# Performance work log

Hardware: AMD Instinct MI355X
Metric: run time of the kernel (lower is better)

## Reference

```python
import jax, jax.numpy as jnp
import numpy as np

N = 200000   # nodes
E = 600000   # edges (E*C = 76.8M floats gathered per layer -> memory bound)
C = 128      # channels
L = 2        # GNN layers
OUT = 1      # head out_channels
SEEDS = 1024


def setup_inputs() -> dict:
    key = jax.random.key(0)
    ks = jax.random.split(key, 8)
    s = 1.0 / np.sqrt(C)
    return {
        "x": jax.random.normal(ks[0], (N, C), jnp.float32),
        "node_time": jax.random.randint(ks[1], (N,), 0, 4),          # times in [0,4)
        "edge_index": jax.random.randint(ks[2], (2, E), 0, N),
        "w_root": jax.random.normal(ks[3], (L, C, C), jnp.float32) * s,
        "w_nbr": jax.random.normal(ks[4], (L, C, C), jnp.float32) * s,
        "bias": jnp.zeros((L, C), jnp.float32),
        "ln_g": jnp.ones((L, C), jnp.float32),
        "ln_b": jnp.zeros((L, C), jnp.float32),
        "head_w": jax.random.normal(ks[5], (C, OUT), jnp.float32) * s,
        "head_b": jnp.zeros((OUT,), jnp.float32),
        "min_timestamp": 0,
        "max_timestamp": 3,
        "update_period": 1,
        "num_seeds": SEEDS,
    }


def _layer_norm(h, g, b):
    mu = h.mean(-1, keepdims=True)
    var = h.var(-1, keepdims=True)
    return (h - mu) * jax.lax.rsqrt(var + 1e-5) * g + b


def reference(x, node_time, edge_index, w_root, w_nbr, bias, ln_g, ln_b,
              head_w, head_b, min_timestamp, max_timestamp, update_period, num_seeds):
    src, dst = edge_index[0], edge_index[1]
    n = x.shape[0]
    n_layers = w_root.shape[0]
    # edge introduction time = max of endpoint times (partition_edges_by_time_dict)
    intro = jnp.maximum(node_time[src], node_time[dst])
    periods = (intro - min_timestamp) // update_period
    P = (max_timestamp - min_timestamp + update_period) // update_period  # static int

    for p in range(P):
        emask = periods == p                     # [E] edges of this time period
        ef = emask.astype(x.dtype)
        ei = emask.astype(jnp.int32)
        # nodes involved in this period's subgraph (appear as src or dst of a period edge)
        cnt = jnp.zeros((n,), jnp.int32).at[src].add(ei).at[dst].add(ei)
        involved = cnt > 0                       # [N]
        # in-degree within the period subgraph (for mean aggregation)
        deg = jax.ops.segment_sum(ef, dst, num_segments=n)
        inv_deg = (1.0 / jnp.maximum(deg, 1.0))[:, None]
        # GraphSAGE on the period subgraph: masked edges == subgraph edges, and the
        # per-node (root/LayerNorm/ReLU) transforms agree with the extracted subgraph.
        h = x
        for l in range(n_layers):
            msg = h[src] * ef[:, None]                               # gather + mask
            agg = jax.ops.segment_sum(msg, dst, num_segments=n) * inv_deg
            h = h @ w_root[l] + agg @ w_nbr[l] + bias[l]
            h = _layer_norm(h, ln_g[l], ln_b[l])
            if l < n_layers - 1:
                h = jax.nn.relu(h)
        # x_dict[node_ids] += out_feats  (scatter-add restricted to involved nodes)
        x = x + jnp.where(involved[:, None], h, jnp.zeros((), x.dtype))

    # head: MLP(channels -> out_channels, num_layers=1) on the seed rows
    return x[:num_seeds] @ head_w + head_b
```

## Files before the change

kernel.cpp:

```cpp
#include <hip/hip_runtime.h>


#define CD 128

typedef __attribute__((ext_vector_type(8))) short s16x8;
typedef __attribute__((ext_vector_type(4))) float f32x4;

static __device__ __forceinline__ unsigned short f2bf(float f) {
  unsigned u = __float_as_uint(f);
  u += 0x7FFF + ((u >> 16) & 1);
  return (unsigned short)(u >> 16);
}
static __device__ __forceinline__ float bf2f(unsigned us) {
  return __uint_as_float(us << 16);
}

__global__ __launch_bounds__(256) void histk(const int* __restrict__ ntime,
    const int* __restrict__ eidx, int* __restrict__ deg_pd,
    unsigned char* __restrict__ inv,
    const int* __restrict__ minp, const int* __restrict__ up, int N, int E) {
  int e = blockIdx.x * 256 + threadIdx.x;
  if (e >= E) return;
  int s = eidx[e], d = eidx[E + e];
  int ts = ntime[s], td = ntime[d];
  int m = ts > td ? ts : td;
  int p = (m - minp[0]) / up[0];
  atomicAdd(&deg_pd[p * N + d], 1);
  inv[(size_t)p * N + s] = 1;
  inv[(size_t)p * N + d] = 1;
}

__global__ __launch_bounds__(256) void compcnt(const unsigned char* __restrict__ inv,
    int* __restrict__ bcnt, int NB2, int N) {
  int i = blockIdx.x * 256 + threadIdx.x;
  int bits = 0;
  if (i < N)
    bits = (int)inv[i] | ((int)inv[N + i] << 1)
         | ((int)inv[2 * (size_t)N + i] << 2) | ((int)inv[3 * (size_t)N + i] << 3);
  int wv = threadIdx.x >> 6;
  int lane = threadIdx.x & 63;
  __shared__ int wcnt[4][4];
#pragma unroll
  for (int p = 0; p < 4; ++p) {
    unsigned long long m = __ballot((bits >> p) & 1);
    if (lane == 0) wcnt[p][wv] = __popcll(m);
  }
  __syncthreads();
  if (threadIdx.x < 4) {
    int p = threadIdx.x;
    bcnt[p * NB2 + blockIdx.x] = wcnt[p][0] + wcnt[p][1] + wcnt[p][2] + wcnt[p][3];
  }
}

__global__ __launch_bounds__(256) void compscat(const unsigned char* __restrict__ inv,
    const int* __restrict__ bcnt, const int* __restrict__ bexc,
    int* __restrict__ nlist, int* __restrict__ cidx, int* __restrict__ ncnt,
    int NB2, int N) {
  int i = blockIdx.x * 256 + threadIdx.x;
  int bits = 0;
  if (i < N)
    bits = (int)inv[i] | ((int)inv[N + i] << 1)
         | ((int)inv[2 * (size_t)N + i] << 2) | ((int)inv[3 * (size_t)N + i] << 3);
  if (blockIdx.x == 0 && threadIdx.x < 4) {
    int p = threadIdx.x;
    ncnt[p] = bexc[p * NB2 + NB2 - 1] + bcnt[p * NB2 + NB2 - 1] - bexc[p * NB2];
  }
  int wv = threadIdx.x >> 6;
  int lane = threadIdx.x & 63;
  unsigned long long lanes_below = (lane == 0) ? 0ull : ((~0ull) >> (64 - lane));
  __shared__ int wcnt[4][4];
  unsigned long long mm[4];
#pragma unroll
  for (int p = 0; p < 4; ++p) {
    mm[p] = __ballot((bits >> p) & 1);
    if (lane == 0) wcnt[p][wv] = __popcll(mm[p]);
  }
  __syncthreads();
#pragma unroll
  for (int p = 0; p < 4; ++p) {
    if (!((bits >> p) & 1)) continue;
    int wpre = (wv > 0 ? wcnt[p][0] : 0) + (wv > 1 ? wcnt[p][1] : 0)
             + (wv > 2 ? wcnt[p][2] : 0);
    int base = bexc[p * NB2 + blockIdx.x] - bexc[p * NB2];
    int pos = base + wpre + __popcll(mm[p] & lanes_below);
    nlist[p * N + pos] = i;
    cidx[p * N + i] = pos;
  }
}

__global__ __launch_bounds__(256) void scan1(const int* __restrict__ in,
    int* __restrict__ out, int* __restrict__ bsums, int M) {
  __shared__ int lds[256];
  int tid = threadIdx.x;
  int base = blockIdx.x * 1024 + tid * 4;
  int v0 = base + 0 < M ? in[base + 0] : 0;
  int v1 = base + 1 < M ? in[base + 1] : 0;
  int v2 = base + 2 < M ? in[base + 2] : 0;
  int v3 = base + 3 < M ? in[base + 3] : 0;
  int s = v0 + v1 + v2 + v3;
  lds[tid] = s;
  __syncthreads();
  for (int off = 1; off < 256; off <<= 1) {
    int t = tid >= off ? lds[tid - off] : 0;
    __syncthreads();
    lds[tid] += t;
    __syncthreads();
  }
  int run = lds[tid] - s;
  if (base + 0 < M) out[base + 0] = run; run += v0;
  if (base + 1 < M) out[base + 1] = run; run += v1;
  if (base + 2 < M) out[base + 2] = run; run += v2;
  if (base + 3 < M) out[base + 3] = run;
  if (tid == 255) bsums[blockIdx.x] = lds[255];
}

__global__ __launch_bounds__(256) void scan2(int* __restrict__ b, int M) {
  __shared__ int lds[256];
  int tid = threadIdx.x;
  int base = tid * 4;
  int v0 = base + 0 < M ? b[base + 0] : 0;
  int v1 = base + 1 < M ? b[base + 1] : 0;
  int v2 = base + 2 < M ? b[base + 2] : 0;
  int v3 = base + 3 < M ? b[base + 3] : 0;
  int s = v0 + v1 + v2 + v3;
  lds[tid] = s;
  __syncthreads();
  for (int off = 1; off < 256; off <<= 1) {
    int t = tid >= off ? lds[tid - off] : 0;
    __syncthreads();
    lds[tid] += t;
    __syncthreads();
  }
  int run = lds[tid] - s;
  if (base + 0 < M) b[base + 0] = run; run += v0;
  if (base + 1 < M) b[base + 1] = run; run += v1;
  if (base + 2 < M) b[base + 2] = run; run += v2;
  if (base + 3 < M) b[base + 3] = run;
}

__global__ __launch_bounds__(256) void scan3(int* __restrict__ out,
    const int* __restrict__ bsums, int M) {
  int add = bsums[blockIdx.x];
  int idx = blockIdx.x * 1024 + threadIdx.x;
#pragma unroll
  for (int k = 0; k < 4; ++k) {
    int i = idx + k * 256;
    if (i < M) out[i] += add;
  }
}

__global__ __launch_bounds__(256) void fillk(const int* __restrict__ ntime,
    const int* __restrict__ eidx, int* __restrict__ row_ptr, int* __restrict__ col,
    const int* __restrict__ minp, const int* __restrict__ up, int N, int E) {
  int e = blockIdx.x * 256 + threadIdx.x;
  if (e >= E) return;
  int s = eidx[e], d = eidx[E + e];
  int ts = ntime[s], td = ntime[d];
  int m = ts > td ? ts : td;
  int p = (m - minp[0]) / up[0];
  int pos = atomicAdd(&row_ptr[p * N + d], 1);
  col[pos] = s;
}

__global__ __launch_bounds__(256) void wprep(const float* __restrict__ wroot,
    const float* __restrict__ wnbr, unsigned short* __restrict__ wt, int total) {
  int t = blockIdx.x * 256 + threadIdx.x;
  if (t >= total) return;
  int l = t >> 12;
  int rem = t & 4095;
  int q = rem >> 7;
  int n = rem & 127;
  const float* src = (q < 16) ? (wroot + l * CD * CD) : (wnbr + l * CD * CD);
  int qh = q & 15;
  unsigned short o[8];
#pragma unroll
  for (int j = 0; j < 8; ++j) {
    int kp = qh * 8 + j;
    int kt = (kp & 7) * 16 + (kp >> 3);
    o[j] = f2bf(src[kt * CD + n]);
  }
  uint4 pk;
  pk.x = (unsigned)o[0] | ((unsigned)o[1] << 16);
  pk.y = (unsigned)o[2] | ((unsigned)o[3] << 16);
  pk.z = (unsigned)o[4] | ((unsigned)o[5] << 16);
  pk.w = (unsigned)o[6] | ((unsigned)o[7] << 16);
  *(uint4*)(wt + (size_t)l * 32768 + ((size_t)q * CD + n) * 8) = pk;
}

__global__ __launch_bounds__(256) void xprep(const float* __restrict__ x,
    unsigned short* __restrict__ xb, float* __restrict__ x32, int nseed, int total) {
  int t = blockIdx.x * 256 + threadIdx.x;
  if (t >= total) return;
  int row = t >> 4, j = t & 15;
  const float* xp = x + (size_t)row * CD + j;
  bool seed = row < nseed;
  float* x3 = x32 + (size_t)row * CD + j;
  unsigned short o[8];
#pragma unroll
  for (int tt = 0; tt < 8; ++tt) {
    float v = xp[tt * 16];
    o[tt] = f2bf(v);
    if (seed) x3[tt * 16] = v;
  }
  uint4 pk;
  pk.x = (unsigned)o[0] | ((unsigned)o[1] << 16);
  pk.y = (unsigned)o[2] | ((unsigned)o[3] << 16);
  pk.z = (unsigned)o[4] | ((unsigned)o[5] << 16);
  pk.w = (unsigned)o[6] | ((unsigned)o[7] << 16);
  *(uint4*)(xb + (size_t)row * CD + j * 8) = pk;
}

__global__ __launch_bounds__(256) void aggk(const unsigned short* __restrict__ hbf,
    unsigned short* __restrict__ aggbf, const int* __restrict__ row_ptr,
    const int* __restrict__ deg_pd, const int* __restrict__ col,
    const int* __restrict__ nlp, const int* __restrict__ pcnt,
    const int* __restrict__ cmap, int p, int N) {
  int cnt = pcnt[0];
  int gi = blockIdx.x * 16 + (threadIdx.x >> 4);
  if (gi >= cnt) return;
  int d = nlp[gi];
  int lane = threadIdx.x & 15;
  int key = p * N + d;
  int dg = deg_pd[key];
  uint4 outv = make_uint4(0u, 0u, 0u, 0u);
  if (dg > 0) {
    int start = row_ptr[key] - dg;
    float a[8];
#pragma unroll
    for (int i = 0; i < 8; ++i) a[i] = 0.f;
    for (int j = 0; j < dg; ++j) {
      int s = col[start + j];
      int r = cmap ? cmap[s] : s;
      uint4 rv = *(const uint4*)(hbf + (size_t)r * CD + lane * 8);
      a[0] += bf2f(rv.x & 0xffffu); a[1] += bf2f(rv.x >> 16);
      a[2] += bf2f(rv.y & 0xffffu); a[3] += bf2f(rv.y >> 16);
      a[4] += bf2f(rv.z & 0xffffu); a[5] += bf2f(rv.z >> 16);
      a[6] += bf2f(rv.w & 0xffffu); a[7] += bf2f(rv.w >> 16);
    }
    float sc = 1.0f / (float)dg;
    outv.x = (unsigned)f2bf(a[0] * sc) | ((unsigned)f2bf(a[1] * sc) << 16);
    outv.y = (unsigned)f2bf(a[2] * sc) | ((unsigned)f2bf(a[3] * sc) << 16);
    outv.z = (unsigned)f2bf(a[4] * sc) | ((unsigned)f2bf(a[5] * sc) << 16);
    outv.w = (unsigned)f2bf(a[6] * sc) | ((unsigned)f2bf(a[7] * sc) << 16);
  }
  *(uint4*)(aggbf + (size_t)gi * CD + lane * 8) = outv;
}

__global__ __launch_bounds__(256, 2) void gemm_mfma(
    const unsigned short* __restrict__ A1, const unsigned short* __restrict__ A2,
    const unsigned short* __restrict__ wt,
    const float* __restrict__ bias, const float* __restrict__ lng,
    const float* __restrict__ lnb,
    unsigned short* __restrict__ hout,
    float* __restrict__ x32, unsigned short* __restrict__ xbf,
    const int* __restrict__ nlp, const int* __restrict__ pcnt,
    int mode, int nseed) {
  int cnt = pcnt[0];
  int rbase = blockIdx.x * 128;
  if (rbase >= cnt) return;

  __shared__ unsigned short Blds[32768];
  {
    const uint4* src = (const uint4*)wt;
    uint4* dst = (uint4*)Blds;
#pragma unroll
    for (int i = 0; i < 16; ++i) dst[threadIdx.x + i * 256] = src[threadIdx.x + i * 256];
  }
  __syncthreads();

  int tid = threadIdx.x;
  int w = tid >> 6;
  int lane = tid & 63;
  int l15 = lane & 15;
  int quad = lane >> 4;

  const unsigned short* base1[2];
  const unsigned short* base2[2];
#pragma unroll
  for (int rt = 0; rt < 2; ++rt) {
    int ii = rbase + w * 32 + rt * 16 + l15;
    ii = ii < cnt ? ii : cnt - 1;
    int arow = (mode == 0) ? nlp[ii] : ii;
    base1[rt] = A1 + (size_t)arow * CD;
    base2[rt] = A2 + (size_t)ii * CD;
  }

  s16x8 af[4][2][2];
#pragma unroll
  for (int kc = 0; kc < 4; ++kc) {
    int koff = (kc & 1) * 64;
#pragma unroll
    for (int ks = 0; ks < 2; ++ks) {
      int kb = (ks * 4 + quad) * 8;
#pragma unroll
      for (int rt = 0; rt < 2; ++rt)
        af[kc][ks][rt] = *(const s16x8*)((kc < 2 ? base1[rt] : base2[rt]) + koff + kb);
    }
  }

  f32x4 acc[2][8];
#pragma unroll
  for (int rt = 0; rt < 2; ++rt)
#pragma unroll
    for (int ct = 0; ct < 8; ++ct) acc[rt][ct] = (f32x4)(0.f);

#pragma unroll
  for (int kc = 0; kc < 4; ++kc) {
#pragma unroll
    for (int ks = 0; ks < 2; ++ks) {
      int q = kc * 8 + ks * 4 + quad;
      s16x8 bfr[8];
#pragma unroll
      for (int ct = 0; ct < 8; ++ct)
        bfr[ct] = *(const s16x8*)&Blds[((size_t)q * CD + l15) * 8 + (size_t)ct * 128];
#pragma unroll
      for (int rt = 0; rt < 2; ++rt)
#pragma unroll
        for (int ct = 0; ct < 8; ++ct)
          acc[rt][ct] = __builtin_amdgcn_mfma_f32_16x16x32_bf16(
              af[kc][ks][rt], bfr[ct], acc[rt][ct], 0, 0, 0);
    }
  }

  float bb[8], gg[8], eb[8];
#pragma unroll
  for (int ct = 0; ct < 8; ++ct) {
    int c = ct * 16 + l15;
    bb[ct] = bias[c]; gg[ct] = lng[c]; eb[ct] = lnb[c];
  }
#pragma unroll
  for (int rt = 0; rt < 2; ++rt) {
#pragma unroll
    for (int reg = 0; reg < 4; ++reg) {
      int ridx = rbase + w * 32 + rt * 16 + quad * 4 + reg;
      float vals[8];
      float s = 0.f, ss = 0.f;
#pragma unroll
      for (int ct = 0; ct < 8; ++ct) {
        float v = acc[rt][ct][reg] + bb[ct];
        vals[ct] = v;
        s += v; ss += v * v;
      }
#pragma unroll
      for (int m = 1; m <= 8; m <<= 1) {
        s  += __shfl_xor(s, m, 64);
        ss += __shfl_xor(ss, m, 64);
      }
      float mu  = s * (1.0f / CD);
      float var = ss * (1.0f / CD) - mu * mu;
      float rs  = rsqrtf(var + 1e-5f);
      if (ridx < cnt) {
        float o[8];
#pragma unroll
        for (int ct = 0; ct < 8; ++ct) o[ct] = (vals[ct] - mu) * rs * gg[ct] + eb[ct];
        if (mode == 0) {
          uint4 pk;
          pk.x = (unsigned)f2bf(fmaxf(o[0], 0.f)) | ((unsigned)f2bf(fmaxf(o[1], 0.f)) << 16);
          pk.y = (unsigned)f2bf(fmaxf(o[2], 0.f)) | ((unsigned)f2bf(fmaxf(o[3], 0.f)) << 16);
          pk.z = (unsigned)f2bf(fmaxf(o[4], 0.f)) | ((unsigned)f2bf(fmaxf(o[5], 0.f)) << 16);
          pk.w = (unsigned)f2bf(fmaxf(o[6], 0.f)) | ((unsigned)f2bf(fmaxf(o[7], 0.f)) << 16);
          *(uint4*)(hout + (size_t)ridx * CD + l15 * 8) = pk;
        } else {
          int node = nlp[ridx];
          unsigned short* xp = xbf + (size_t)node * CD + l15 * 8;
          uint4 old = *(const uint4*)xp;
          float xn0 = bf2f(old.x & 0xffffu) + o[0], xn1 = bf2f(old.x >> 16) + o[1];
          float xn2 = bf2f(old.y & 0xffffu) + o[2], xn3 = bf2f(old.y >> 16) + o[3];
          float xn4 = bf2f(old.z & 0xffffu) + o[4], xn5 = bf2f(old.z >> 16) + o[5];
          float xn6 = bf2f(old.w & 0xffffu) + o[6], xn7 = bf2f(old.w >> 16) + o[7];
          uint4 pk;
          pk.x = (unsigned)f2bf(xn0) | ((unsigned)f2bf(xn1) << 16);
          pk.y = (unsigned)f2bf(xn2) | ((unsigned)f2bf(xn3) << 16);
          pk.z = (unsigned)f2bf(xn4) | ((unsigned)f2bf(xn5) << 16);
          pk.w = (unsigned)f2bf(xn6) | ((unsigned)f2bf(xn7) << 16);
          *(uint4*)xp = pk;
          if (node < nseed) {
            float* x3 = x32 + (size_t)node * CD + l15;
#pragma unroll
            for (int ct = 0; ct < 8; ++ct) x3[ct * 16] += o[ct];
          }
        }
      }
    }
  }
}

__global__ __launch_bounds__(256) void headk(const float* __restrict__ x,
    const float* __restrict__ hw, const float* __restrict__ hb,
    float* __restrict__ out, int seeds) {
  int wave = threadIdx.x >> 6;
  int lane = threadIdx.x & 63;
  int row = blockIdx.x * 4 + wave;
  if (row >= seeds) return;
  const float* xp = x + (size_t)row * CD;
  float v = xp[lane] * hw[lane] + xp[64 + lane] * hw[64 + lane];
#pragma unroll
  for (int m = 1; m < 64; m <<= 1) v += __shfl_xor(v, m, 64);
  if (lane == 0) out[row] = v + hb[0];
}

extern "C" void kernel_launch(void* const* d_in, const int* in_sizes, int n_in,
                              void* d_out, int out_size, void* d_ws, size_t ws_size,
                              hipStream_t stream) {
  const float* x     = (const float*)d_in[0];
  const int*   ntime = (const int*)d_in[1];
  const int*   eidx  = (const int*)d_in[2];
  const float* wroot = (const float*)d_in[3];
  const float* wnbr  = (const float*)d_in[4];
  const float* bias  = (const float*)d_in[5];
  const float* lng   = (const float*)d_in[6];
  const float* lnb   = (const float*)d_in[7];
  const float* headw = (const float*)d_in[8];
  const float* headb = (const float*)d_in[9];
  const int*   minp  = (const int*)d_in[10];
  const int*   up    = (const int*)d_in[12];

  int N = in_sizes[0] / CD;
  int E = in_sizes[2] / 2;
  const int P = 4;
  int M = P * N;
  int nseed = out_size;

  size_t off = 0;
  auto alloc = [&](size_t bytes) {
    void* p = (char*)d_ws + off;
    off += (bytes + 255) & ~(size_t)255;
    return p;
  };
  unsigned short* x_bf   = (unsigned short*)alloc((size_t)N * CD * 2);
  unsigned short* h_bf   = (unsigned short*)alloc((size_t)N * CD * 2);
  unsigned short* agg_bf = (unsigned short*)alloc((size_t)N * CD * 2);
  float*          x32    = (float*)alloc((size_t)nseed * CD * 4);
  unsigned short* wt     = (unsigned short*)alloc(2 * 32768 * 2);
  int* deg_pd   = (int*)alloc((size_t)M * 4);
  int* row_ptr  = (int*)alloc((size_t)M * 4);
  int* col      = (int*)alloc((size_t)E * 4);
  unsigned char* inv = (unsigned char*)alloc((size_t)M);
  int* nlist    = (int*)alloc((size_t)M * 4);
  int* cidx     = (int*)alloc((size_t)M * 4);
  int* ncnt     = (int*)alloc(256);
  int* bsums    = (int*)alloc(4096);

  int NB2 = (N + 255) / 256;
  int M2 = 4 * NB2;
  int* bcnt = (int*)alloc((size_t)M2 * 4);
  int* bexc = (int*)alloc((size_t)M2 * 4);
  (void)ws_size;

  hipMemsetAsync(deg_pd, 0, (size_t)M * 4, stream);
  hipMemsetAsync(inv, 0, (size_t)M, stream);

  int egrid = (E + 255) / 256;
  int NB = (M + 1023) / 1024;
  int NBc = (M2 + 1023) / 1024;
  int ggrid = (N + 127) / 128;
  int agrid = (N + 15) / 16;

  xprep<<<(N * 16 + 255) / 256, 256, 0, stream>>>(x, x_bf, x32, nseed, N * 16);
  wprep<<<(8192 + 255) / 256, 256, 0, stream>>>(wroot, wnbr, wt, 8192);
  histk<<<egrid, 256, 0, stream>>>(ntime, eidx, deg_pd, inv, minp, up, N, E);

  compcnt<<<NB2, 256, 0, stream>>>(inv, bcnt, NB2, N);
  scan1<<<NBc, 256, 0, stream>>>(bcnt, bexc, bsums, M2);
  scan2<<<1, 256, 0, stream>>>(bsums, NBc);
  scan3<<<NBc, 256, 0, stream>>>(bexc, bsums, M2);
  compscat<<<NB2, 256, 0, stream>>>(inv, bcnt, bexc, nlist, cidx, ncnt, NB2, N);

  scan1<<<NB, 256, 0, stream>>>(deg_pd, row_ptr, bsums, M);
  scan2<<<1, 256, 0, stream>>>(bsums, NB);
  scan3<<<NB, 256, 0, stream>>>(row_ptr, bsums, M);
  fillk<<<egrid, 256, 0, stream>>>(ntime, eidx, row_ptr, col, minp, up, N, E);

  for (int p = 0; p < P; ++p) {
    const int* nlp = nlist + (size_t)p * N;
    const int* pc  = ncnt + p;
    const int* cm  = cidx + (size_t)p * N;
    aggk<<<agrid, 256, 0, stream>>>(x_bf, agg_bf, row_ptr, deg_pd, col, nlp, pc,
        nullptr, p, N);
    gemm_mfma<<<ggrid, 256, 0, stream>>>(x_bf, agg_bf, wt,
        bias, lng, lnb, h_bf, nullptr, nullptr, nlp, pc, 0, nseed);
    aggk<<<agrid, 256, 0, stream>>>(h_bf, agg_bf, row_ptr, deg_pd, col, nlp, pc,
        cm, p, N);
    gemm_mfma<<<ggrid, 256, 0, stream>>>(h_bf, agg_bf, wt + 32768,
        bias + CD, lng + CD, lnb + CD, nullptr, x32, x_bf, nlp, pc, 1, nseed);
  }
  headk<<<(nseed + 3) / 4, 256, 0, stream>>>(x32, headw, headb, (float*)d_out, nseed);
}
```

Baseline: 654.2 us.

## Fuse neighbor mean aggregation into MFMA GEMM and precompute compacted column indices

```diff
diff --git a/kernel.cpp b/kernel.cpp
--- a/kernel.cpp
+++ b/kernel.cpp
@@ -13,6 +13,18 @@
 }
 static __device__ __forceinline__ float bf2f(unsigned us) {
   return __uint_as_float(us << 16);
+}
+static __device__ __forceinline__ void acc8(float* a, uint4 v) {
+  a[0] += bf2f(v.x & 0xffffu); a[1] += bf2f(v.x >> 16);
+  a[2] += bf2f(v.y & 0xffffu); a[3] += bf2f(v.y >> 16);
+  a[4] += bf2f(v.z & 0xffffu); a[5] += bf2f(v.z >> 16);
+  a[6] += bf2f(v.w & 0xffffu); a[7] += bf2f(v.w >> 16);
+}
+static __device__ __forceinline__ s16x8 pack8(const float* a, float sc) {
+  s16x8 r;
+#pragma unroll
+  for (int j = 0; j < 8; ++j) r[j] = (short)f2bf(a[j] * sc);
+  return r;
 }
 
 __global__ __launch_bounds__(256) void histk(const int* __restrict__ ntime,
@@ -162,6 +174,15 @@
   col[pos] = s;
 }
 
+__global__ __launch_bounds__(256) void remapk(const int* __restrict__ col,
+    int* __restrict__ col2, const int* __restrict__ cidx,
+    const int* __restrict__ row_ptr, int N, int E) {
+  int i = blockIdx.x * 256 + threadIdx.x;
+  if (i >= E) return;
+  int p = (i >= row_ptr[N - 1]) + (i >= row_ptr[2 * N - 1]) + (i >= row_ptr[3 * N - 1]);
+  col2[i] = cidx[(size_t)p * N + col[i]];
+}
+
 __global__ __launch_bounds__(256) void wprep(const float* __restrict__ wroot,
     const float* __restrict__ wnbr, unsigned short* __restrict__ wt, int total) {
   int t = blockIdx.x * 256 + threadIdx.x;
@@ -210,51 +231,17 @@
   *(uint4*)(xb + (size_t)row * CD + j * 8) = pk;
 }
 
-__global__ __launch_bounds__(256) void aggk(const unsigned short* __restrict__ hbf,
-    unsigned short* __restrict__ aggbf, const int* __restrict__ row_ptr,
-    const int* __restrict__ deg_pd, const int* __restrict__ col,
-    const int* __restrict__ nlp, const int* __restrict__ pcnt,
-    const int* __restrict__ cmap, int p, int N) {
-  int cnt = pcnt[0];
-  int gi = blockIdx.x * 16 + (threadIdx.x >> 4);
-  if (gi >= cnt) return;
-  int d = nlp[gi];
-  int lane = threadIdx.x & 15;
-  int key = p * N + d;
-  int dg = deg_pd[key];
-  uint4 outv = make_uint4(0u, 0u, 0u, 0u);
-  if (dg > 0) {
-    int start = row_ptr[key] - dg;
-    float a[8];
-#pragma unroll
-    for (int i = 0; i < 8; ++i) a[i] = 0.f;
-    for (int j = 0; j < dg; ++j) {
-      int s = col[start + j];
-      int r = cmap ? cmap[s] : s;
-      uint4 rv = *(const uint4*)(hbf + (size_t)r * CD + lane * 8);
-      a[0] += bf2f(rv.x & 0xffffu); a[1] += bf2f(rv.x >> 16);
-      a[2] += bf2f(rv.y & 0xffffu); a[3] += bf2f(rv.y >> 16);
-      a[4] += bf2f(rv.z & 0xffffu); a[5] += bf2f(rv.z >> 16);
-      a[6] += bf2f(rv.w & 0xffffu); a[7] += bf2f(rv.w >> 16);
-    }
-    float sc = 1.0f / (float)dg;
-    outv.x = (unsigned)f2bf(a[0] * sc) | ((unsigned)f2bf(a[1] * sc) << 16);
-    outv.y = (unsigned)f2bf(a[2] * sc) | ((unsigned)f2bf(a[3] * sc) << 16);
-    outv.z = (unsigned)f2bf(a[4] * sc) | ((unsigned)f2bf(a[5] * sc) << 16);
-    outv.w = (unsigned)f2bf(a[6] * sc) | ((unsigned)f2bf(a[7] * sc) << 16);
-  }
-  *(uint4*)(aggbf + (size_t)gi * CD + lane * 8) = outv;
-}
-
-__global__ __launch_bounds__(256, 2) void gemm_mfma(
-    const unsigned short* __restrict__ A1, const unsigned short* __restrict__ A2,
+__global__ __launch_bounds__(256, 2) void gemm_fused(
+    const unsigned short* __restrict__ feat,
     const unsigned short* __restrict__ wt,
     const float* __restrict__ bias, const float* __restrict__ lng,
     const float* __restrict__ lnb,
     unsigned short* __restrict__ hout,
     float* __restrict__ x32, unsigned short* __restrict__ xbf,
     const int* __restrict__ nlp, const int* __restrict__ pcnt,
-    int mode, int nseed) {
+    const int* __restrict__ deg_pd, const int* __restrict__ row_ptr,
+    const int* __restrict__ cols,
+    int p, int N, int mode, int nseed) {
   int cnt = pcnt[0];
   int rbase = blockIdx.x * 128;
   if (rbase >= cnt) return;
@@ -266,7 +253,6 @@
 #pragma unroll
     for (int i = 0; i < 16; ++i) dst[threadIdx.x + i * 256] = src[threadIdx.x + i * 256];
   }
-  __syncthreads();
 
   int tid = threadIdx.x;
   int w = tid >> 6;
@@ -274,29 +260,55 @@
   int l15 = lane & 15;
   int quad = lane >> 4;
 
-  const unsigned short* base1[2];
-  const unsigned short* base2[2];
+  int dg_[2], st_[2];
+  const unsigned short* b1[2];
 #pragma unroll
   for (int rt = 0; rt < 2; ++rt) {
     int ii = rbase + w * 32 + rt * 16 + l15;
     ii = ii < cnt ? ii : cnt - 1;
-    int arow = (mode == 0) ? nlp[ii] : ii;
-    base1[rt] = A1 + (size_t)arow * CD;
-    base2[rt] = A2 + (size_t)ii * CD;
+    int node = nlp[ii];
+    int key = p * N + node;
+    int dg = deg_pd[key];
+    dg_[rt] = dg;
+    st_[rt] = row_ptr[key] - dg;
+    b1[rt] = feat + (size_t)(mode == 0 ? node : ii) * CD;
   }
 
   s16x8 af[4][2][2];
 #pragma unroll
-  for (int kc = 0; kc < 4; ++kc) {
-    int koff = (kc & 1) * 64;
+  for (int kc = 0; kc < 2; ++kc)
 #pragma unroll
     for (int ks = 0; ks < 2; ++ks) {
-      int kb = (ks * 4 + quad) * 8;
+      int off = kc * 64 + (ks * 4 + quad) * 8;
 #pragma unroll
       for (int rt = 0; rt < 2; ++rt)
-        af[kc][ks][rt] = *(const s16x8*)((kc < 2 ? base1[rt] : base2[rt]) + koff + kb);
+        af[kc][ks][rt] = *(const s16x8*)(b1[rt] + off);
     }
-  }
+
+  int cb = quad * 8;
+#pragma unroll
+  for (int rt = 0; rt < 2; ++rt) {
+    float a0[8], a1[8], a2[8], a3[8];
+#pragma unroll
+    for (int j = 0; j < 8; ++j) { a0[j] = 0.f; a1[j] = 0.f; a2[j] = 0.f; a3[j] = 0.f; }
+    int dg = dg_[rt], st = st_[rt];
+    for (int j = 0; j < dg; ++j) {
+      int r = cols[st + j];
+      const unsigned short* rp = feat + (size_t)r * CD;
+      uint4 v0 = *(const uint4*)(rp + cb);
+      uint4 v1 = *(const uint4*)(rp + cb + 32);
+      uint4 v2 = *(const uint4*)(rp + cb + 64);
+      uint4 v3 = *(const uint4*)(rp + cb + 96);
+      acc8(a0, v0); acc8(a1, v1); acc8(a2, v2); acc8(a3, v3);
+    }
+    float sc = dg > 0 ? 1.0f / (float)dg : 0.f;
+    af[2][0][rt] = pack8(a0, sc);
+    af[2][1][rt] = pack8(a1, sc);
+    af[3][0][rt] = pack8(a2, sc);
+    af[3][1][rt] = pack8(a3, sc);
+  }
+
+  __syncthreads();
 
   f32x4 acc[2][8];
 #pragma unroll
@@ -427,14 +439,14 @@
     off += (bytes + 255) & ~(size_t)255;
     return p;
   };
-  unsigned short* x_bf   = (unsigned short*)alloc((size_t)N * CD * 2);
-  unsigned short* h_bf   = (unsigned short*)alloc((size_t)N * CD * 2);
-  unsigned short* agg_bf = (unsigned short*)alloc((size_t)N * CD * 2);
-  float*          x32    = (float*)alloc((size_t)nseed * CD * 4);
-  unsigned short* wt     = (unsigned short*)alloc(2 * 32768 * 2);
+  unsigned short* x_bf = (unsigned short*)alloc((size_t)N * CD * 2);
+  unsigned short* h_bf = (unsigned short*)alloc((size_t)N * CD * 2);
+  float*          x32  = (float*)alloc((size_t)nseed * CD * 4);
+  unsigned short* wt   = (unsigned short*)alloc(2 * 32768 * 2);
   int* deg_pd   = (int*)alloc((size_t)M * 4);
   int* row_ptr  = (int*)alloc((size_t)M * 4);
   int* col      = (int*)alloc((size_t)E * 4);
+  int* col2     = (int*)alloc((size_t)E * 4);
   unsigned char* inv = (unsigned char*)alloc((size_t)M);
   int* nlist    = (int*)alloc((size_t)M * 4);
   int* cidx     = (int*)alloc((size_t)M * 4);
@@ -454,7 +466,6 @@
   int NB = (M + 1023) / 1024;
   int NBc = (M2 + 1023) / 1024;
   int ggrid = (N + 127) / 128;
-  int agrid = (N + 15) / 16;
 
   xprep<<<(N * 16 + 255) / 256, 256, 0, stream>>>(x, x_bf, x32, nseed, N * 16);
   wprep<<<(8192 + 255) / 256, 256, 0, stream>>>(wroot, wnbr, wt, 8192);
@@ -470,19 +481,17 @@
   scan2<<<1, 256, 0, stream>>>(bsums, NB);
   scan3<<<NB, 256, 0, stream>>>(row_ptr, bsums, M);
   fillk<<<egrid, 256, 0, stream>>>(ntime, eidx, row_ptr, col, minp, up, N, E);
+  remapk<<<egrid, 256, 0, stream>>>(col, col2, cidx, row_ptr, N, E);
 
   for (int p = 0; p < P; ++p) {
     const int* nlp = nlist + (size_t)p * N;
     const int* pc  = ncnt + p;
-    const int* cm  = cidx + (size_t)p * N;
-    aggk<<<agrid, 256, 0, stream>>>(x_bf, agg_bf, row_ptr, deg_pd, col, nlp, pc,
-        nullptr, p, N);
-    gemm_mfma<<<ggrid, 256, 0, stream>>>(x_bf, agg_bf, wt,
-        bias, lng, lnb, h_bf, nullptr, nullptr, nlp, pc, 0, nseed);
-    aggk<<<agrid, 256, 0, stream>>>(h_bf, agg_bf, row_ptr, deg_pd, col, nlp, pc,
-        cm, p, N);
-    gemm_mfma<<<ggrid, 256, 0, stream>>>(h_bf, agg_bf, wt + 32768,
-        bias + CD, lng + CD, lnb + CD, nullptr, x32, x_bf, nlp, pc, 1, nseed);
+    gemm_fused<<<ggrid, 256, 0, stream>>>(x_bf, wt,
+        bias, lng, lnb, h_bf, nullptr, nullptr, nlp, pc,
+        deg_pd, row_ptr, col, p, N, 0, nseed);
+    gemm_fused<<<ggrid, 256, 0, stream>>>(h_bf, wt + 32768,
+        bias + CD, lng + CD, lnb + CD, nullptr, x32, x_bf, nlp, pc,
+        deg_pd, row_ptr, col2, p, N, 1, nseed);
   }
   headk<<<(nseed + 3) / 4, 256, 0, stream>>>(x32, headw, headb, (float*)d_out, nseed);
 }
```

Measured after the change: 621.0 us. -5.1%, faster.
